# Kernel tuning notes

Measured on AMD Instinct MI355X. Metric: run time of the kernel, lower is better.

## Reference

```python
import jax, jax.numpy as jnp
import numpy as np

T = 64       # tasks per observation sequence
B = 65536    # number of observation sequences
C = 32       # capabilityRepresentationSize
NUM_TASKS = 6


def setup_inputs() -> dict:
    key = jax.random.key(0)
    k1, k2, k3 = jax.random.split(key, 3)
    # obsMatrix as in requirementTransform: col 0 zeros, cols 1..5 ~ U(0,1) with seed 0
    rng = np.random.RandomState(0)
    obsMatrix = np.zeros((C, NUM_TASKS), dtype=np.float32)
    obsMatrix[:, 1:NUM_TASKS] = rng.rand(C, NUM_TASKS - 1)
    # performance code: 0 -> (0,0) no-op, 1 -> (0,1) success, 2 -> (1,0) failure; (1,1) forbidden
    code = jax.random.randint(k1, (T, B), 0, 3)
    inptasksperf = jnp.stack([(code == 2).astype(jnp.int32),
                              (code == 1).astype(jnp.int32)], axis=-1)  # [T,B,2]
    tasksobsids = jax.random.randint(k2, (T, B, 1), 0, NUM_TASKS)
    taskspredids = jax.random.randint(k3, (B, 1), 0, NUM_TASKS)
    return {"inptasksperf": inptasksperf,
            "tasksobsids": tasksobsids,
            "taskspredids": taskspredids,
            "obsMatrix": jnp.asarray(obsMatrix)}


def reference(inptasksperf, tasksobsids, taskspredids, obsMatrix):
    # success/failure booleans per (t, b)
    p0 = inptasksperf[..., 0] != 0
    p1 = inptasksperf[..., 1] != 0
    success = jnp.logical_and(~p0, p1)   # [T,B]
    failure = jnp.logical_and(p0, ~p1)   # [T,B]
    # gather observed capability vectors: obsMatrix[:, id] -> [T,B,C]
    cap = obsMatrix.T[tasksobsids[..., 0]]

    def step(mean, xs):
        c, s, f = xs  # c: [B,C], s/f: [B]
        # success: elementwise running max; failure: elementwise running min
        mean = jnp.where(s[:, None], jnp.maximum(mean, c), mean)
        mean = jnp.where(f[:, None], jnp.minimum(mean, c), mean)
        return mean, None

    mean0 = jnp.zeros((B, C), dtype=obsMatrix.dtype)
    mean, _ = jax.lax.scan(step, mean0, (cap, success, failure))  # [B,C]

    # computeTrust: 1 iff required[i] <= mean[i] for all i
    required = obsMatrix.T[taskspredids[:, 0]]  # [B,C]
    trust = jnp.all(required <= mean, axis=1).astype(obsMatrix.dtype)[:, None]  # [B,1]
    return trust
```

## Files before the change

### kernel.cpp

```cpp
#include <hip/hip_runtime.h>

namespace {

constexpr int T = 64;
constexpr int B = 65536;
constexpr int C = 32;
constexpr int NT = 6;
constexpr int WAVES = 8;
constexpr int BLOCK = WAVES * 64;
constexpr int CHUNK = T / WAVES;
constexpr int SEQS = 256;
constexpr int QS = 8;

typedef int v4i __attribute__((ext_vector_type(4)));

#if __has_builtin(__builtin_amdgcn_make_buffer_rsrc) && \
    __has_builtin(__builtin_amdgcn_raw_buffer_load_b128)
#define USE_BUF 1
#else
#define USE_BUF 0
#endif

__global__ __launch_bounds__(BLOCK) void trust_kernel(
    const int2* __restrict__ perf,
    const int*  __restrict__ obsids,
    const int*  __restrict__ predids,
    const float* __restrict__ obsM,
    float* __restrict__ out)
{
    __shared__ float    MT[NT * C];
    __shared__ unsigned Qtab[7 * QS];
    __shared__ uint2    sab[WAVES][SEQS];

    const int tid  = threadIdx.x;
    const int lane = tid & 63;
    const int w    = tid >> 6;

    if (tid < C * NT) {
        const int c = tid / NT, j = tid - c * NT;
        MT[j * C + c] = obsM[tid];
    }
    __syncthreads();
    {
        const int half = lane >> 5;
        const int c    = lane & 31;
        for (int k = w; k <= 20; k += WAVES) {
            const int e   = 2 * k + half;
            const int id  = e / 6;
            const int pid = e - id * 6;
            const float val = (id < 6) ? MT[id * C + c] : 0.0f;
            const float req = MT[pid * C + c];
            const unsigned long long bal = __ballot(req <= val);
            if (c == 0) {
                Qtab[id * QS + pid] =
                    (unsigned)(half ? (bal >> 32) : (bal & 0xFFFFFFFFull));
            }
        }
    }
    __syncthreads();

    const int sbase = blockIdx.x * SEQS;
    const int tb    = w * CHUNK;

    v4i pfA[CHUNK], pfB[CHUNK], idv[CHUNK];
#if USE_BUF
    const auto rs_perf = __builtin_amdgcn_make_buffer_rsrc(
        (void*)perf, (short)0, T * B * 8, 0x00020000);
    const auto rs_ids = __builtin_amdgcn_make_buffer_rsrc(
        (void*)obsids, (short)0, T * B * 4, 0x00020000);
    const auto rs_pid = __builtin_amdgcn_make_buffer_rsrc(
        (void*)predids, (short)0, B * 4, 0x00020000);
#pragma unroll
    for (int k = 0; k < CHUNK; ++k) {
        const int e = (tb + k) * B + sbase;
        pfA[k] = (v4i)__builtin_amdgcn_raw_buffer_load_b128(
            rs_perf, e * 8 + 32 * lane, 0, 0x12);
        pfB[k] = (v4i)__builtin_amdgcn_raw_buffer_load_b128(
            rs_perf, e * 8 + 32 * lane + 16, 0, 0x12);
        idv[k] = (v4i)__builtin_amdgcn_raw_buffer_load_b128(
            rs_ids, e * 4 + 16 * lane, 0, 0x12);
    }
    const v4i pid4 = (v4i)__builtin_amdgcn_raw_buffer_load_b128(
        rs_pid, sbase * 4 + 16 * lane, 0, 0x12);
#else
#pragma unroll
    for (int k = 0; k < CHUNK; ++k) {
        const int e = (tb + k) * B + sbase;
        pfA[k] = __builtin_nontemporal_load(((const v4i*)perf) + (e >> 1) + 2 * lane);
        pfB[k] = __builtin_nontemporal_load(((const v4i*)perf) + (e >> 1) + 2 * lane + 1);
        idv[k] = __builtin_nontemporal_load(((const v4i*)obsids) + (e >> 2) + lane);
    }
    const v4i pid4 = __builtin_nontemporal_load(
        ((const v4i*)predids) + (sbase >> 2) + lane);
#endif

    unsigned a0 = ~0u, b0 = 0u, a1 = ~0u, b1 = 0u;
    unsigned a2 = ~0u, b2 = 0u, a3 = ~0u, b3 = 0u;

#define STEP(px, py, idq, pidq, aA, bB)                                     \
    do {                                                                    \
        const unsigned Q_  = Qtab[(idq) * QS + (pidq)];                     \
        const unsigned A_  = ((px) != 0) ? Q_ : 0xFFFFFFFFu;                \
        const unsigned Bv_ = ((py) != 0) ? Q_ : 0u;                         \
        aA = aA & A_;                                                       \
        bB = (bB & A_) | Bv_;                                               \
    } while (0)

#pragma unroll
    for (int k = 0; k < CHUNK; ++k) {
        STEP(pfA[k].x, pfA[k].y, idv[k].x, pid4.x, a0, b0);
        STEP(pfA[k].z, pfA[k].w, idv[k].y, pid4.y, a1, b1);
        STEP(pfB[k].x, pfB[k].y, idv[k].z, pid4.z, a2, b2);
        STEP(pfB[k].z, pfB[k].w, idv[k].w, pid4.w, a3, b3);
    }
#undef STEP

    const int s0 = 4 * lane;
    sab[w][s0 + 0] = make_uint2(a0, b0);
    sab[w][s0 + 1] = make_uint2(a1, b1);
    sab[w][s0 + 2] = make_uint2(a2, b2);
    sab[w][s0 + 3] = make_uint2(a3, b3);
    __syncthreads();

    if (tid < SEQS) {
        uint2 c0 = sab[0][tid];
        unsigned ca = c0.x, cb = c0.y;
#pragma unroll
        for (int wv = 1; wv < WAVES; ++wv) {
            const uint2 c2 = sab[wv][tid];
            cb = (cb & c2.x) | c2.y;
            ca = ca & c2.x;
        }
        const int pid = __builtin_nontemporal_load(predids + sbase + tid);
        const unsigned Winit = Qtab[6 * QS + pid];
        const unsigned W = (Winit & ca) | cb;
        __builtin_nontemporal_store((W == 0xFFFFFFFFu) ? 1.0f : 0.0f,
                                    out + sbase + tid);
    }
}

}

extern "C" void kernel_launch(void* const* d_in, const int* in_sizes, int n_in,
                              void* d_out, int out_size, void* d_ws, size_t ws_size,
                              hipStream_t stream) {
    const int2*  perf    = (const int2*)d_in[0];
    const int*   obsids  = (const int*)d_in[1];
    const int*   predids = (const int*)d_in[2];
    const float* obsM    = (const float*)d_in[3];
    float*       out     = (float*)d_out;

    dim3 grid(B / SEQS), block(BLOCK);
    trust_kernel<<<grid, block, 0, stream>>>(perf, obsids, predids, obsM, out);
}
```

Before: 13.88 us.

## Halve sequences per block and issue global loads before table setup

Each block now handles 128 sequences instead of 256, so each lane processes 2 sequences with 128-bit perf and 64-bit id loads. The grid doubles, which gives more parallelism and uses fewer registers per thread. The global loads are also moved ahead of the shared-memory table construction, so their latency overlaps the LDS setup and ballot work. The cost is smaller per-lane loads and twice as many blocks, each repeating the table setup.

```diff
diff --git a/kernel.cpp b/kernel.cpp
--- a/kernel.cpp
+++ b/kernel.cpp
@@ -9,13 +9,15 @@
 constexpr int WAVES = 8;
 constexpr int BLOCK = WAVES * 64;
 constexpr int CHUNK = T / WAVES;
-constexpr int SEQS = 256;
+constexpr int SEQS = 128;
 constexpr int QS = 8;
 
 typedef int v4i __attribute__((ext_vector_type(4)));
+typedef int v2i __attribute__((ext_vector_type(2)));
 
-#if __has_builtin(__builtin_amdgcn_make_buffer_rsrc) && \
-    __has_builtin(__builtin_amdgcn_raw_buffer_load_b128)
+#if __has_builtin(__builtin_amdgcn_make_buffer_rsrc) &&   \
+    __has_builtin(__builtin_amdgcn_raw_buffer_load_b128) && \
+    __has_builtin(__builtin_amdgcn_raw_buffer_load_b64)
 #define USE_BUF 1
 #else
 #define USE_BUF 0
@@ -35,6 +37,39 @@
     const int tid  = threadIdx.x;
     const int lane = tid & 63;
     const int w    = tid >> 6;
+
+    const int sbase = blockIdx.x * SEQS;
+    const int tb    = w * CHUNK;
+
+    v4i pf2[CHUNK];
+    v2i idv[CHUNK];
+#if USE_BUF
+    const auto rs_perf = __builtin_amdgcn_make_buffer_rsrc(
+        (void*)perf, (short)0, T * B * 8, 0x00020000);
+    const auto rs_ids = __builtin_amdgcn_make_buffer_rsrc(
+        (void*)obsids, (short)0, T * B * 4, 0x00020000);
+    const auto rs_pid = __builtin_amdgcn_make_buffer_rsrc(
+        (void*)predids, (short)0, B * 4, 0x00020000);
+#pragma unroll
+    for (int k = 0; k < CHUNK; ++k) {
+        const int e = (tb + k) * B + sbase;
+        pf2[k] = (v4i)__builtin_amdgcn_raw_buffer_load_b128(
+            rs_perf, e * 8 + 16 * lane, 0, 0x12);
+        idv[k] = (v2i)__builtin_amdgcn_raw_buffer_load_b64(
+            rs_ids, e * 4 + 8 * lane, 0, 0x12);
+    }
+    const v2i pid2 = (v2i)__builtin_amdgcn_raw_buffer_load_b64(
+        rs_pid, sbase * 4 + 8 * lane, 0, 0x12);
+#else
+#pragma unroll
+    for (int k = 0; k < CHUNK; ++k) {
+        const int e = (tb + k) * B + sbase;
+        pf2[k] = __builtin_nontemporal_load(((const v4i*)perf) + (e >> 1) + lane);
+        idv[k] = __builtin_nontemporal_load(((const v2i*)obsids) + (e >> 1) + lane);
+    }
+    const v2i pid2 = __builtin_nontemporal_load(
+        ((const v2i*)predids) + (sbase >> 1) + lane);
+#endif
 
     if (tid < C * NT) {
         const int c = tid / NT, j = tid - c * NT;
@@ -59,43 +94,7 @@
     }
     __syncthreads();
 
-    const int sbase = blockIdx.x * SEQS;
-    const int tb    = w * CHUNK;
-
-    v4i pfA[CHUNK], pfB[CHUNK], idv[CHUNK];
-#if USE_BUF
-    const auto rs_perf = __builtin_amdgcn_make_buffer_rsrc(
-        (void*)perf, (short)0, T * B * 8, 0x00020000);
-    const auto rs_ids = __builtin_amdgcn_make_buffer_rsrc(
-        (void*)obsids, (short)0, T * B * 4, 0x00020000);
-    const auto rs_pid = __builtin_amdgcn_make_buffer_rsrc(
-        (void*)predids, (short)0, B * 4, 0x00020000);
-#pragma unroll
-    for (int k = 0; k < CHUNK; ++k) {
-        const int e = (tb + k) * B + sbase;
-        pfA[k] = (v4i)__builtin_amdgcn_raw_buffer_load_b128(
-            rs_perf, e * 8 + 32 * lane, 0, 0x12);
-        pfB[k] = (v4i)__builtin_amdgcn_raw_buffer_load_b128(
-            rs_perf, e * 8 + 32 * lane + 16, 0, 0x12);
-        idv[k] = (v4i)__builtin_amdgcn_raw_buffer_load_b128(
-            rs_ids, e * 4 + 16 * lane, 0, 0x12);
-    }
-    const v4i pid4 = (v4i)__builtin_amdgcn_raw_buffer_load_b128(
-        rs_pid, sbase * 4 + 16 * lane, 0, 0x12);
-#else
-#pragma unroll
-    for (int k = 0; k < CHUNK; ++k) {
-        const int e = (tb + k) * B + sbase;
-        pfA[k] = __builtin_nontemporal_load(((const v4i*)perf) + (e >> 1) + 2 * lane);
-        pfB[k] = __builtin_nontemporal_load(((const v4i*)perf) + (e >> 1) + 2 * lane + 1);
-        idv[k] = __builtin_nontemporal_load(((const v4i*)obsids) + (e >> 2) + lane);
-    }
-    const v4i pid4 = __builtin_nontemporal_load(
-        ((const v4i*)predids) + (sbase >> 2) + lane);
-#endif
-
     unsigned a0 = ~0u, b0 = 0u, a1 = ~0u, b1 = 0u;
-    unsigned a2 = ~0u, b2 = 0u, a3 = ~0u, b3 = 0u;
 
 #define STEP(px, py, idq, pidq, aA, bB)                                     \
     do {                                                                    \
@@ -108,18 +107,14 @@
 
 #pragma unroll
     for (int k = 0; k < CHUNK; ++k) {
-        STEP(pfA[k].x, pfA[k].y, idv[k].x, pid4.x, a0, b0);
-        STEP(pfA[k].z, pfA[k].w, idv[k].y, pid4.y, a1, b1);
-        STEP(pfB[k].x, pfB[k].y, idv[k].z, pid4.z, a2, b2);
-        STEP(pfB[k].z, pfB[k].w, idv[k].w, pid4.w, a3, b3);
+        STEP(pf2[k].x, pf2[k].y, idv[k].x, pid2.x, a0, b0);
+        STEP(pf2[k].z, pf2[k].w, idv[k].y, pid2.y, a1, b1);
     }
 #undef STEP
 
-    const int s0 = 4 * lane;
+    const int s0 = 2 * lane;
     sab[w][s0 + 0] = make_uint2(a0, b0);
     sab[w][s0 + 1] = make_uint2(a1, b1);
-    sab[w][s0 + 2] = make_uint2(a2, b2);
-    sab[w][s0 + 3] = make_uint2(a3, b3);
     __syncthreads();
 
     if (tid < SEQS) {
```

New measurement: 12.15 us. 12.4% less time.
